# Performance work log

Measured on AMD Instinct MI355X. Metric: run time of the kernel, lower is better.

## Reference

```python
import jax, jax.numpy as jnp
import numpy as np

B, N, C, H = 4, 1024, 768, 12
HD = C // H

def setup_inputs() -> dict:
    key = jax.random.key(0)
    ks = jax.random.split(key, 6)
    s = 0.02
    return {
        "x": jax.random.normal(ks[0], (B, N, C), jnp.float32),
        "attn_bias": jax.random.normal(ks[1], (H, N, N), jnp.float32),
        "qkv_w": jax.random.normal(ks[2], (C, 3 * C), jnp.float32) * s,
        "qkv_b": jax.random.normal(ks[3], (3 * C,), jnp.float32) * s,
        "proj_w": jax.random.normal(ks[4], (C, C), jnp.float32) * s,
        "proj_b": jax.random.normal(ks[5], (C,), jnp.float32) * s,
    }

def reference(x, attn_bias, qkv_w, qkv_b, proj_w, proj_b):
    b, n, c = x.shape
    scale = HD ** -0.5
    qkv = x @ qkv_w + qkv_b                      # [B,N,3C]
    qkv = qkv.reshape(b, n, 3, H, HD)
    q = qkv[:, :, 0].transpose(0, 2, 1, 3)       # [B,H,N,HD]
    k = qkv[:, :, 1].transpose(0, 2, 1, 3)
    v = qkv[:, :, 2].transpose(0, 2, 1, 3)
    attn = jnp.einsum('bhqd,bhkd->bhqk', q, k) * scale
    attn = attn + attn_bias[None]                # broadcast over batch
    attn = jax.nn.softmax(attn, axis=-1)
    y = jnp.einsum('bhqk,bhkd->bhqd', attn, v)   # [B,H,N,HD]
    y = y.transpose(0, 2, 1, 3).reshape(b, n, c)
    return y @ proj_w + proj_b
```

## Files before the change

kernel.cpp:

```cpp
#include <hip/hip_runtime.h>
#include <hip/hip_bf16.h>

constexpr int BATCH = 4;
constexpr int NSEQ  = 1024;
constexpr int CDIM  = 768;
constexpr int NHEAD = 12;
constexpr int HDIM  = 64;
constexpr int MTOT  = BATCH * NSEQ;
constexpr int QKVN  = 3 * CDIM;

typedef __bf16 bf16x8 __attribute__((ext_vector_type(8)));
typedef float  f32x4  __attribute__((ext_vector_type(4)));

__device__ __forceinline__ unsigned short f2bf(float f) {
    unsigned u = __builtin_bit_cast(unsigned, f);
    unsigned r = u + 0x7FFFu + ((u >> 16) & 1u);
    return (unsigned short)(r >> 16);
}

#define GLOAD_LDS16(gp, lp)                                                    \
    __builtin_amdgcn_global_load_lds(                                          \
        (const __attribute__((address_space(1))) void*)(gp),                   \
        (__attribute__((address_space(3))) void*)(lp), 16, 0, 0)

__global__ __launch_bounds__(256) void cvt_f32_bf16(
    const float* __restrict__ in, unsigned short* __restrict__ out, int n4)
{
    int i = blockIdx.x * 256 + threadIdx.x;
    if (i < n4) {
        float4 a = reinterpret_cast<const float4*>(in)[i];
        ushort4 h;
        h.x = f2bf(a.x); h.y = f2bf(a.y); h.z = f2bf(a.z); h.w = f2bf(a.w);
        reinterpret_cast<ushort4*>(out)[i] = h;
    }
}

__global__ __launch_bounds__(256) void tcvt_f32_bf16(
    const float* __restrict__ in, unsigned short* __restrict__ out, int R, int C)
{
    __shared__ unsigned short t[32][33];
    const int c0 = blockIdx.x * 32, r0 = blockIdx.y * 32;
    const int tc = threadIdx.x & 31, tr = threadIdx.x >> 5;
    #pragma unroll
    for (int i = 0; i < 4; i++)
        t[tc][tr + 8 * i] = f2bf(in[(size_t)(r0 + tr + 8 * i) * C + c0 + tc]);
    __syncthreads();
    #pragma unroll
    for (int i = 0; i < 4; i++)
        out[(size_t)(c0 + tr + 8 * i) * R + r0 + tc] = t[tr + 8 * i][tc];
}

__global__ __launch_bounds__(256) void qkv_gemm(
    const unsigned short* __restrict__ xb,
    const unsigned short* __restrict__ wt,
    const float* __restrict__ bias,
    unsigned short* __restrict__ qbuf, unsigned short* __restrict__ kbuf,
    unsigned short* __restrict__ vtbuf)
{
    __shared__ unsigned short As[128 * 32];
    __shared__ unsigned short Bs[128 * 32];
    const int tid  = threadIdx.x;
    const int lane = tid & 63;
    const int wid  = tid >> 6;
    const int wm = (wid >> 1) * 64, wn = (wid & 1) * 64;
    const int g = lane >> 4, li = lane & 15;
    const int m0 = blockIdx.y * 128;
    const int n0 = blockIdx.x * 128;
    const int srow = lane >> 2;
    const int scol = (lane & 3) * 8;

    f32x4 acc[4][4];
    #pragma unroll
    for (int i = 0; i < 4; i++)
        #pragma unroll
        for (int j = 0; j < 4; j++) acc[i][j] = f32x4{0.f, 0.f, 0.f, 0.f};

    for (int k0 = 0; k0 < CDIM; k0 += 32) {
        __syncthreads();
        #pragma unroll
        for (int c = 0; c < 2; c++) {
            int row = wid * 32 + c * 16 + srow;
            GLOAD_LDS16(&xb[(size_t)(m0 + row) * CDIM + k0 + scol],
                        &As[(wid * 32 + c * 16) * 32]);
            GLOAD_LDS16(&wt[(size_t)(n0 + row) * CDIM + k0 + scol],
                        &Bs[(wid * 32 + c * 16) * 32]);
        }
        __syncthreads();
        bf16x8 a[4], b[4];
        #pragma unroll
        for (int mt = 0; mt < 4; mt++)
            a[mt] = *reinterpret_cast<const bf16x8*>(&As[(wm + 16 * mt + li) * 32 + 8 * g]);
        #pragma unroll
        for (int nt = 0; nt < 4; nt++)
            b[nt] = *reinterpret_cast<const bf16x8*>(&Bs[(wn + 16 * nt + li) * 32 + 8 * g]);
        #pragma unroll
        for (int mt = 0; mt < 4; mt++)
            #pragma unroll
            for (int nt = 0; nt < 4; nt++)
                acc[mt][nt] = __builtin_amdgcn_mfma_f32_16x16x32_bf16(a[mt], b[nt], acc[mt][nt], 0, 0, 0);
    }

    #pragma unroll
    for (int mt = 0; mt < 4; mt++) {
        #pragma unroll
        for (int nt = 0; nt < 4; nt++) {
            int col  = n0 + wn + 16 * nt + li;
            int tsel = col / CDIM;
            int rem  = col - tsel * CDIM;
            int h_ = rem >> 6, d = rem & 63;
            float bv = bias[col];
            #pragma unroll
            for (int r = 0; r < 4; r++) {
                int m  = m0 + wm + 16 * mt + 4 * g + r;
                int b_ = m >> 10, s = m & 1023;
                unsigned short hv = f2bf(acc[mt][nt][r] + bv);
                if (tsel == 0)
                    qbuf[(((size_t)b_ * NHEAD + h_) * NSEQ + s) * HDIM + d] = hv;
                else if (tsel == 1)
                    kbuf[(((size_t)b_ * NHEAD + h_) * NSEQ + s) * HDIM + d] = hv;
                else
                    vtbuf[(((size_t)b_ * NHEAD + h_) * HDIM + d) * NSEQ + s] = hv;
            }
        }
    }
}

__global__ __launch_bounds__(256, 3) void attn_kernel(
    const unsigned short* __restrict__ qbuf,
    const unsigned short* __restrict__ kbuf,
    const unsigned short* __restrict__ vtbuf,
    const float* __restrict__ bias,
    unsigned short* __restrict__ ybuf)
{
    __shared__ unsigned short Ks[128][72];
    __shared__ unsigned short Vs[64][136];
    __shared__ unsigned short Ps[4][16][136];

    const int tid  = threadIdx.x;
    const int lane = tid & 63;
    const int wid  = tid >> 6;
    const int g = lane >> 4, li = lane & 15;
    const int bh = blockIdx.y;
    const int b_ = bh / NHEAD, h_ = bh % NHEAD;
    const int qw = blockIdx.x * 64 + wid * 16;
    const float scale = 0.125f;

    const unsigned short* qb = qbuf + (size_t)bh * NSEQ * HDIM;
    const unsigned short* kb = kbuf + (size_t)bh * NSEQ * HDIM;
    const unsigned short* vb = vtbuf + (size_t)bh * HDIM * NSEQ;
    const float* bb = bias + (size_t)h_ * NSEQ * NSEQ;

    bf16x8 qf[2];
    #pragma unroll
    for (int dd = 0; dd < 2; dd++)
        qf[dd] = *reinterpret_cast<const bf16x8*>(&qb[(size_t)(qw + li) * HDIM + 32 * dd + 8 * g]);

    f32x4 oacc[4];
    #pragma unroll
    for (int dt = 0; dt < 4; dt++) oacc[dt] = f32x4{0.f, 0.f, 0.f, 0.f};
    float lpart[4] = {0.f, 0.f, 0.f, 0.f};

    for (int k0 = 0; k0 < NSEQ; k0 += 128) {
        float bv[8][4];
        #pragma unroll
        for (int kt = 0; kt < 8; kt++)
            #pragma unroll
            for (int r = 0; r < 4; r++)
                bv[kt][r] = bb[(size_t)(qw + 4 * g + r) * NSEQ + k0 + 16 * kt + li];

        __syncthreads();
        #pragma unroll
        for (int i = 0; i < 4; i++) {
            int j = tid * 4 + i;
            int row = j >> 3, c = (j & 7) * 8;
            *reinterpret_cast<int4*>(&Ks[row][c]) =
                *reinterpret_cast<const int4*>(&kb[(size_t)(k0 + row) * HDIM + c]);
        }
        #pragma unroll
        for (int i = 0; i < 4; i++) {
            int j = tid * 4 + i;
            int row = j >> 4, c = (j & 15) * 8;
            *reinterpret_cast<int4*>(&Vs[row][c]) =
                *reinterpret_cast<const int4*>(&vb[(size_t)row * NSEQ + k0 + c]);
        }
        __syncthreads();

        f32x4 sacc[8];
        #pragma unroll
        for (int kt = 0; kt < 8; kt++) sacc[kt] = f32x4{0.f, 0.f, 0.f, 0.f};
        #pragma unroll
        for (int kt = 0; kt < 8; kt++)
            #pragma unroll
            for (int dd = 0; dd < 2; dd++) {
                bf16x8 kf = *reinterpret_cast<const bf16x8*>(&Ks[16 * kt + li][32 * dd + 8 * g]);
                sacc[kt] = __builtin_amdgcn_mfma_f32_16x16x32_bf16(qf[dd], kf, sacc[kt], 0, 0, 0);
            }

        #pragma unroll
        for (int kt = 0; kt < 8; kt++)
            #pragma unroll
            for (int r = 0; r < 4; r++) {
                float pv = __expf(sacc[kt][r] * scale + bv[kt][r]);
                lpart[r] += pv;
                Ps[wid][4 * g + r][16 * kt + li] = f2bf(pv);
            }

        #pragma unroll
        for (int kk = 0; kk < 4; kk++) {
            bf16x8 pf = *reinterpret_cast<const bf16x8*>(&Ps[wid][li][32 * kk + 8 * g]);
            #pragma unroll
            for (int dt = 0; dt < 4; dt++) {
                bf16x8 vf = *reinterpret_cast<const bf16x8*>(&Vs[16 * dt + li][32 * kk + 8 * g]);
                oacc[dt] = __builtin_amdgcn_mfma_f32_16x16x32_bf16(pf, vf, oacc[dt], 0, 0, 0);
            }
        }
    }

    float linv[4];
    #pragma unroll
    for (int r = 0; r < 4; r++) {
        float s = lpart[r];
        s += __shfl_xor(s, 1);
        s += __shfl_xor(s, 2);
        s += __shfl_xor(s, 4);
        s += __shfl_xor(s, 8);
        linv[r] = 1.f / s;
    }
    #pragma unroll
    for (int dt = 0; dt < 4; dt++)
        #pragma unroll
        for (int r = 0; r < 4; r++) {
            float o = oacc[dt][r] * linv[r];
            int s = qw + 4 * g + r;
            ybuf[((size_t)b_ * NSEQ + s) * CDIM + h_ * HDIM + 16 * dt + li] = f2bf(o);
        }
}

__global__ __launch_bounds__(256) void proj_gemm(
    const unsigned short* __restrict__ yb,
    const unsigned short* __restrict__ pwt,
    const float* __restrict__ bias, float* __restrict__ out)
{
    __shared__ unsigned short As[128 * 32];
    __shared__ unsigned short Bs[128 * 32];
    const int tid  = threadIdx.x;
    const int lane = tid & 63;
    const int wid  = tid >> 6;
    const int wm = (wid >> 1) * 64, wn = (wid & 1) * 64;
    const int g = lane >> 4, li = lane & 15;
    const int m0 = blockIdx.y * 128;
    const int n0 = blockIdx.x * 128;
    const int srow = lane >> 2;
    const int scol = (lane & 3) * 8;

    f32x4 acc[4][4];
    #pragma unroll
    for (int i = 0; i < 4; i++)
        #pragma unroll
        for (int j = 0; j < 4; j++) acc[i][j] = f32x4{0.f, 0.f, 0.f, 0.f};

    for (int k0 = 0; k0 < CDIM; k0 += 32) {
        __syncthreads();
        #pragma unroll
        for (int c = 0; c < 2; c++) {
            int row = wid * 32 + c * 16 + srow;
            GLOAD_LDS16(&yb[(size_t)(m0 + row) * CDIM + k0 + scol],
                        &As[(wid * 32 + c * 16) * 32]);
            GLOAD_LDS16(&pwt[(size_t)(n0 + row) * CDIM + k0 + scol],
                        &Bs[(wid * 32 + c * 16) * 32]);
        }
        __syncthreads();
        bf16x8 a[4], b[4];
        #pragma unroll
        for (int mt = 0; mt < 4; mt++)
            a[mt] = *reinterpret_cast<const bf16x8*>(&As[(wm + 16 * mt + li) * 32 + 8 * g]);
        #pragma unroll
        for (int nt = 0; nt < 4; nt++)
            b[nt] = *reinterpret_cast<const bf16x8*>(&Bs[(wn + 16 * nt + li) * 32 + 8 * g]);
        #pragma unroll
        for (int mt = 0; mt < 4; mt++)
            #pragma unroll
            for (int nt = 0; nt < 4; nt++)
                acc[mt][nt] = __builtin_amdgcn_mfma_f32_16x16x32_bf16(a[mt], b[nt], acc[mt][nt], 0, 0, 0);
    }

    #pragma unroll
    for (int mt = 0; mt < 4; mt++)
        #pragma unroll
        for (int nt = 0; nt < 4; nt++) {
            int col = n0 + wn + 16 * nt + li;
            float bv = bias[col];
            #pragma unroll
            for (int r = 0; r < 4; r++) {
                int m = m0 + wm + 16 * mt + 4 * g + r;
                out[(size_t)m * CDIM + col] = acc[mt][nt][r] + bv;
            }
        }
}

extern "C" void kernel_launch(void* const* d_in, const int* in_sizes, int n_in,
                              void* d_out, int out_size, void* d_ws, size_t ws_size,
                              hipStream_t stream) {
    const float* x         = (const float*)d_in[0];
    const float* attn_bias = (const float*)d_in[1];
    const float* qkv_w     = (const float*)d_in[2];
    const float* qkv_b     = (const float*)d_in[3];
    const float* proj_w    = (const float*)d_in[4];
    const float* proj_b    = (const float*)d_in[5];
    float* out = (float*)d_out;

    const size_t per = (size_t)BATCH * NHEAD * NSEQ * HDIM;
    unsigned short* qbuf  = (unsigned short*)d_ws;
    unsigned short* kbuf  = qbuf + per;
    unsigned short* vtbuf = kbuf + per;
    unsigned short* xb    = vtbuf + per;
    unsigned short* qwt   = xb + per;
    unsigned short* pwt   = qwt + (size_t)QKVN * CDIM;
    unsigned short* ybuf  = xb;

    cvt_f32_bf16<<<(MTOT * CDIM / 4 + 255) / 256, 256, 0, stream>>>(
        x, xb, MTOT * CDIM / 4);
    tcvt_f32_bf16<<<dim3(QKVN / 32, CDIM / 32), 256, 0, stream>>>(
        qkv_w, qwt, CDIM, QKVN);
    tcvt_f32_bf16<<<dim3(CDIM / 32, CDIM / 32), 256, 0, stream>>>(
        proj_w, pwt, CDIM, CDIM);

    qkv_gemm<<<dim3(QKVN / 128, MTOT / 128), 256, 0, stream>>>(
        xb, qwt, qkv_b, qbuf, kbuf, vtbuf);
    attn_kernel<<<dim3(NSEQ / 64, BATCH * NHEAD), 256, 0, stream>>>(
        qbuf, kbuf, vtbuf, attn_bias, ybuf);
    proj_gemm<<<dim3(CDIM / 128, MTOT / 128), 256, 0, stream>>>(
        ybuf, pwt, proj_b, out);
}
```

Before: 114.2 us.

## Prefetch next K/V/bias tile into registers and swizzle attention block order

The attention kernel now loads the next 128-key tile of K, V and the bias into registers while the current tile's MFMAs run, using double-buffered bias registers and a fully unrolled key loop. The grid becomes a flat 768-block launch with a swizzle that maps consecutive block IDs across different (batch, head) pairs. The swizzle probably spreads work across XCDs so blocks sharing the same head's bias and K/V land together for cache reuse. The cost is much higher register pressure (two 32-float bias sets plus 8 int4 prefetch registers), which may cut occupancy below the launch_bounds target of 3.

```diff
diff --git a/kernel.cpp b/kernel.cpp
--- a/kernel.cpp
+++ b/kernel.cpp
@@ -140,9 +140,13 @@
     const int lane = tid & 63;
     const int wid  = tid >> 6;
     const int g = lane >> 4, li = lane & 15;
-    const int bh = blockIdx.y;
+
+    const int lin = blockIdx.x;
+    const int swz = (lin & 7) * 96 + (lin >> 3);
+    const int qtile = swz & 15;
+    const int bh    = swz >> 4;
     const int b_ = bh / NHEAD, h_ = bh % NHEAD;
-    const int qw = blockIdx.x * 64 + wid * 16;
+    const int qw = qtile * 64 + wid * 16;
     const float scale = 0.125f;
 
     const unsigned short* qb = qbuf + (size_t)bh * NSEQ * HDIM;
@@ -160,30 +164,49 @@
     for (int dt = 0; dt < 4; dt++) oacc[dt] = f32x4{0.f, 0.f, 0.f, 0.f};
     float lpart[4] = {0.f, 0.f, 0.f, 0.f};
 
-    for (int k0 = 0; k0 < NSEQ; k0 += 128) {
-        float bv[8][4];
-        #pragma unroll
-        for (int kt = 0; kt < 8; kt++)
-            #pragma unroll
-            for (int r = 0; r < 4; r++)
-                bv[kt][r] = bb[(size_t)(qw + 4 * g + r) * NSEQ + k0 + 16 * kt + li];
-
-        __syncthreads();
-        #pragma unroll
-        for (int i = 0; i < 4; i++) {
-            int j = tid * 4 + i;
-            int row = j >> 3, c = (j & 7) * 8;
-            *reinterpret_cast<int4*>(&Ks[row][c]) =
-                *reinterpret_cast<const int4*>(&kb[(size_t)(k0 + row) * HDIM + c]);
-        }
-        #pragma unroll
-        for (int i = 0; i < 4; i++) {
-            int j = tid * 4 + i;
-            int row = j >> 4, c = (j & 15) * 8;
-            *reinterpret_cast<int4*>(&Vs[row][c]) =
-                *reinterpret_cast<const int4*>(&vb[(size_t)row * NSEQ + k0 + c]);
-        }
-        __syncthreads();
+    const int krow = tid >> 1, kcol = (tid & 1) * 32;
+    const int vrow = tid >> 2, vcol = (tid & 3) * 32;
+    int4 kreg[4], vreg[4];
+    float bv[2][8][4];
+
+    #pragma unroll
+    for (int i = 0; i < 4; i++) {
+        kreg[i] = *reinterpret_cast<const int4*>(&kb[(size_t)krow * HDIM + kcol + i * 8]);
+        vreg[i] = *reinterpret_cast<const int4*>(&vb[(size_t)vrow * NSEQ + vcol + i * 8]);
+    }
+    #pragma unroll
+    for (int kt = 0; kt < 8; kt++)
+        #pragma unroll
+        for (int r = 0; r < 4; r++)
+            bv[0][kt][r] = bb[(size_t)(qw + 4 * g + r) * NSEQ + 16 * kt + li];
+
+    #pragma unroll
+    for (int t = 0; t < 8; ++t) {
+        const int k0 = t * 128;
+        __syncthreads();
+        #pragma unroll
+        for (int i = 0; i < 4; i++)
+            *reinterpret_cast<int4*>(&Ks[krow][kcol + i * 8]) = kreg[i];
+        #pragma unroll
+        for (int i = 0; i < 4; i++)
+            *reinterpret_cast<int4*>(&Vs[vrow][vcol + i * 8]) = vreg[i];
+        __syncthreads();
+
+        if (t < 7) {
+            #pragma unroll
+            for (int i = 0; i < 4; i++) {
+                kreg[i] = *reinterpret_cast<const int4*>(
+                    &kb[(size_t)(k0 + 128 + krow) * HDIM + kcol + i * 8]);
+                vreg[i] = *reinterpret_cast<const int4*>(
+                    &vb[(size_t)vrow * NSEQ + k0 + 128 + vcol + i * 8]);
+            }
+            #pragma unroll
+            for (int kt = 0; kt < 8; kt++)
+                #pragma unroll
+                for (int r = 0; r < 4; r++)
+                    bv[(t + 1) & 1][kt][r] =
+                        bb[(size_t)(qw + 4 * g + r) * NSEQ + k0 + 128 + 16 * kt + li];
+        }
 
         f32x4 sacc[8];
         #pragma unroll
@@ -200,7 +223,7 @@
         for (int kt = 0; kt < 8; kt++)
             #pragma unroll
             for (int r = 0; r < 4; r++) {
-                float pv = __expf(sacc[kt][r] * scale + bv[kt][r]);
+                float pv = __expf(sacc[kt][r] * scale + bv[t & 1][kt][r]);
                 lpart[r] += pv;
                 Ps[wid][4 * g + r][16 * kt + li] = f2bf(pv);
             }
@@ -327,7 +350,7 @@
 
     qkv_gemm<<<dim3(QKVN / 128, MTOT / 128), 256, 0, stream>>>(
         xb, qwt, qkv_b, qbuf, kbuf, vtbuf);
-    attn_kernel<<<dim3(NSEQ / 64, BATCH * NHEAD), 256, 0, stream>>>(
+    attn_kernel<<<768, 256, 0, stream>>>(
         qbuf, kbuf, vtbuf, attn_bias, ybuf);
     proj_gemm<<<dim3(CDIM / 128, MTOT / 128), 256, 0, stream>>>(
         ybuf, pwt, proj_b, out);
```

Result: slower. 231.6 us (+102.8%).

## Transpose S tile for vectorized bias loads and remap blocks for bias reuse

Applied to the files above, without the earlier changes.

Swaps the MFMA operand order so each lane owns one query row and four consecutive keys. The bias can then be read as float4 vectors and P written as packed ushort4 stores, and the row-sum reduction drops to two cross-group shuffles. The grid is flattened and remapped so the four batch instances sharing a head's bias tile run close together, which should improve L2/MALL reuse of the large fp32 bias. The mapping hardcodes 768 blocks and 8-way XCD interleaving, and adds a shuffle-based gather of the row sums.

```diff
diff --git a/kernel.cpp b/kernel.cpp
--- a/kernel.cpp
+++ b/kernel.cpp
@@ -140,9 +140,15 @@
     const int lane = tid & 63;
     const int wid  = tid >> 6;
     const int g = lane >> 4, li = lane & 15;
-    const int bh = blockIdx.y;
-    const int b_ = bh / NHEAD, h_ = bh % NHEAD;
-    const int qw = blockIdx.x * 64 + wid * 16;
+
+    const int lin = blockIdx.x;
+    const int s   = (lin & 7) * 96 + (lin >> 3);
+    const int b_    = s & 3;
+    const int hq    = s >> 2;
+    const int qtile = hq & 15;
+    const int h_    = hq >> 4;
+    const int bh    = b_ * NHEAD + h_;
+    const int qw = qtile * 64 + wid * 16;
     const float scale = 0.125f;
 
     const unsigned short* qb = qbuf + (size_t)bh * NSEQ * HDIM;
@@ -158,15 +164,14 @@
     f32x4 oacc[4];
     #pragma unroll
     for (int dt = 0; dt < 4; dt++) oacc[dt] = f32x4{0.f, 0.f, 0.f, 0.f};
-    float lpart[4] = {0.f, 0.f, 0.f, 0.f};
+    float lpart = 0.f;
 
     for (int k0 = 0; k0 < NSEQ; k0 += 128) {
-        float bv[8][4];
+        f32x4 bv[8];
         #pragma unroll
         for (int kt = 0; kt < 8; kt++)
-            #pragma unroll
-            for (int r = 0; r < 4; r++)
-                bv[kt][r] = bb[(size_t)(qw + 4 * g + r) * NSEQ + k0 + 16 * kt + li];
+            bv[kt] = *reinterpret_cast<const f32x4*>(
+                &bb[(size_t)(qw + li) * NSEQ + k0 + 16 * kt + 4 * g]);
 
         __syncthreads();
         #pragma unroll
@@ -193,17 +198,20 @@
             #pragma unroll
             for (int dd = 0; dd < 2; dd++) {
                 bf16x8 kf = *reinterpret_cast<const bf16x8*>(&Ks[16 * kt + li][32 * dd + 8 * g]);
-                sacc[kt] = __builtin_amdgcn_mfma_f32_16x16x32_bf16(qf[dd], kf, sacc[kt], 0, 0, 0);
+                sacc[kt] = __builtin_amdgcn_mfma_f32_16x16x32_bf16(kf, qf[dd], sacc[kt], 0, 0, 0);
             }
 
         #pragma unroll
-        for (int kt = 0; kt < 8; kt++)
-            #pragma unroll
-            for (int r = 0; r < 4; r++) {
-                float pv = __expf(sacc[kt][r] * scale + bv[kt][r]);
-                lpart[r] += pv;
-                Ps[wid][4 * g + r][16 * kt + li] = f2bf(pv);
-            }
+        for (int kt = 0; kt < 8; kt++) {
+            ushort4 pk;
+            float p0 = __expf(sacc[kt][0] * scale + bv[kt][0]);
+            float p1 = __expf(sacc[kt][1] * scale + bv[kt][1]);
+            float p2 = __expf(sacc[kt][2] * scale + bv[kt][2]);
+            float p3 = __expf(sacc[kt][3] * scale + bv[kt][3]);
+            lpart += p0 + p1 + p2 + p3;
+            pk.x = f2bf(p0); pk.y = f2bf(p1); pk.z = f2bf(p2); pk.w = f2bf(p3);
+            *reinterpret_cast<ushort4*>(&Ps[wid][li][16 * kt + 4 * g]) = pk;
+        }
 
         #pragma unroll
         for (int kk = 0; kk < 4; kk++) {
@@ -216,23 +224,20 @@
         }
     }
 
+    lpart += __shfl_xor(lpart, 16);
+    lpart += __shfl_xor(lpart, 32);
     float linv[4];
     #pragma unroll
-    for (int r = 0; r < 4; r++) {
-        float s = lpart[r];
-        s += __shfl_xor(s, 1);
-        s += __shfl_xor(s, 2);
-        s += __shfl_xor(s, 4);
-        s += __shfl_xor(s, 8);
-        linv[r] = 1.f / s;
-    }
+    for (int r = 0; r < 4; r++)
+        linv[r] = 1.f / __shfl(lpart, 4 * g + r);
+
     #pragma unroll
     for (int dt = 0; dt < 4; dt++)
         #pragma unroll
         for (int r = 0; r < 4; r++) {
             float o = oacc[dt][r] * linv[r];
-            int s = qw + 4 * g + r;
-            ybuf[((size_t)b_ * NSEQ + s) * CDIM + h_ * HDIM + 16 * dt + li] = f2bf(o);
+            int sq = qw + 4 * g + r;
+            ybuf[((size_t)b_ * NSEQ + sq) * CDIM + h_ * HDIM + 16 * dt + li] = f2bf(o);
         }
 }
 
@@ -327,7 +332,7 @@
 
     qkv_gemm<<<dim3(QKVN / 128, MTOT / 128), 256, 0, stream>>>(
         xb, qwt, qkv_b, qbuf, kbuf, vtbuf);
-    attn_kernel<<<dim3(NSEQ / 64, BATCH * NHEAD), 256, 0, stream>>>(
+    attn_kernel<<<768, 256, 0, stream>>>(
         qbuf, kbuf, vtbuf, attn_bias, ybuf);
     proj_gemm<<<dim3(CDIM / 128, MTOT / 128), 256, 0, stream>>>(
         ybuf, pwt, proj_b, out);
```

Measured after the change: 119.3 us. +4.5%, slower.

## Compute transposed scores to keep P in registers and drop LDS round-trip

Applied to the files above, without the earlier changes.

The attention kernel now computes S^T (K as the A operand, Q as B), so each lane's score accumulators line up with the A-operand layout of the P·V MFMA. P is packed to bf16 in registers instead of going through the shared Ps buffer. K rows are permuted when stored to LDS so the transposed layout matches. The softmax scale is folded into Q in the QKV GEMM epilogue, the bias loads become vectorized f32x4 reads along rows, and occupancy is raised to 4 blocks per SM. Together these remove LDS traffic and per-element scale multiplies, at the cost of a tricky lane/row permutation that must exactly match the MFMA operand layout.

```diff
diff --git a/kernel.cpp b/kernel.cpp
--- a/kernel.cpp
+++ b/kernel.cpp
@@ -16,6 +16,10 @@
     unsigned u = __builtin_bit_cast(unsigned, f);
     unsigned r = u + 0x7FFFu + ((u >> 16) & 1u);
     return (unsigned short)(r >> 16);
+}
+
+__device__ __forceinline__ unsigned pack_bf16(float lo, float hi) {
+    return (unsigned)f2bf(lo) | ((unsigned)f2bf(hi) << 16);
 }
 
 #define GLOAD_LDS16(gp, lp)                                                    \
@@ -109,11 +113,12 @@
             int rem  = col - tsel * CDIM;
             int h_ = rem >> 6, d = rem & 63;
             float bv = bias[col];
+            float sc = (tsel == 0) ? 0.125f : 1.0f;
             #pragma unroll
             for (int r = 0; r < 4; r++) {
                 int m  = m0 + wm + 16 * mt + 4 * g + r;
                 int b_ = m >> 10, s = m & 1023;
-                unsigned short hv = f2bf(acc[mt][nt][r] + bv);
+                unsigned short hv = f2bf((acc[mt][nt][r] + bv) * sc);
                 if (tsel == 0)
                     qbuf[(((size_t)b_ * NHEAD + h_) * NSEQ + s) * HDIM + d] = hv;
                 else if (tsel == 1)
@@ -125,16 +130,15 @@
     }
 }
 
-__global__ __launch_bounds__(256, 3) void attn_kernel(
+__global__ __launch_bounds__(256, 4) void attn_kernel(
     const unsigned short* __restrict__ qbuf,
     const unsigned short* __restrict__ kbuf,
     const unsigned short* __restrict__ vtbuf,
     const float* __restrict__ bias,
     unsigned short* __restrict__ ybuf)
 {
-    __shared__ unsigned short Ks[128][72];
-    __shared__ unsigned short Vs[64][136];
-    __shared__ unsigned short Ps[4][16][136];
+    __shared__ unsigned short Ks[128 * 72];
+    __shared__ unsigned short Vs[64 * 136];
 
     const int tid  = threadIdx.x;
     const int lane = tid & 63;
@@ -143,13 +147,25 @@
     const int bh = blockIdx.y;
     const int b_ = bh / NHEAD, h_ = bh % NHEAD;
     const int qw = blockIdx.x * 64 + wid * 16;
-    const float scale = 0.125f;
 
     const unsigned short* qb = qbuf + (size_t)bh * NSEQ * HDIM;
     const unsigned short* kb = kbuf + (size_t)bh * NSEQ * HDIM;
     const unsigned short* vb = vtbuf + (size_t)bh * HDIM * NSEQ;
     const float* bb = bias + (size_t)h_ * NSEQ * NSEQ;
 
+    int ksrc[4], ksoff[4], vsrc[4], vsoff[4];
+    #pragma unroll
+    for (int i = 0; i < 4; i++) {
+        int j = tid * 4 + i;
+        int kr = j >> 3, kc = (j & 7) * 8;
+        int kp = (kr & 0x63) | ((kr & 4) << 2) | ((kr & 0x18) >> 1);
+        ksrc[i] = kr * HDIM + kc;
+        ksoff[i] = kp * 72 + kc;
+        int vr = j >> 4, vc = (j & 15) * 8;
+        vsrc[i] = vr * NSEQ + vc;
+        vsoff[i] = vr * 136 + vc;
+    }
+
     bf16x8 qf[2];
     #pragma unroll
     for (int dd = 0; dd < 2; dd++)
@@ -158,81 +174,78 @@
     f32x4 oacc[4];
     #pragma unroll
     for (int dt = 0; dt < 4; dt++) oacc[dt] = f32x4{0.f, 0.f, 0.f, 0.f};
-    float lpart[4] = {0.f, 0.f, 0.f, 0.f};
+    float lpart = 0.f;
 
     for (int k0 = 0; k0 < NSEQ; k0 += 128) {
-        float bv[8][4];
-        #pragma unroll
-        for (int kt = 0; kt < 8; kt++)
-            #pragma unroll
-            for (int r = 0; r < 4; r++)
-                bv[kt][r] = bb[(size_t)(qw + 4 * g + r) * NSEQ + k0 + 16 * kt + li];
+        f32x4 bvlo[4], bvhi[4];
+        #pragma unroll
+        for (int kk = 0; kk < 4; kk++) {
+            const float* bp = &bb[(size_t)(qw + li) * NSEQ + k0 + 32 * kk + 8 * g];
+            bvlo[kk] = *reinterpret_cast<const f32x4*>(bp);
+            bvhi[kk] = *reinterpret_cast<const f32x4*>(bp + 4);
+        }
 
         __syncthreads();
         #pragma unroll
         for (int i = 0; i < 4; i++) {
-            int j = tid * 4 + i;
-            int row = j >> 3, c = (j & 7) * 8;
-            *reinterpret_cast<int4*>(&Ks[row][c]) =
-                *reinterpret_cast<const int4*>(&kb[(size_t)(k0 + row) * HDIM + c]);
-        }
-        #pragma unroll
-        for (int i = 0; i < 4; i++) {
-            int j = tid * 4 + i;
-            int row = j >> 4, c = (j & 15) * 8;
-            *reinterpret_cast<int4*>(&Vs[row][c]) =
-                *reinterpret_cast<const int4*>(&vb[(size_t)row * NSEQ + k0 + c]);
-        }
-        __syncthreads();
-
-        f32x4 sacc[8];
-        #pragma unroll
-        for (int kt = 0; kt < 8; kt++) sacc[kt] = f32x4{0.f, 0.f, 0.f, 0.f};
-        #pragma unroll
-        for (int kt = 0; kt < 8; kt++)
+            *reinterpret_cast<int4*>(&Ks[ksoff[i]]) =
+                *reinterpret_cast<const int4*>(&kb[(size_t)k0 * HDIM + ksrc[i]]);
+            *reinterpret_cast<int4*>(&Vs[vsoff[i]]) =
+                *reinterpret_cast<const int4*>(&vb[(size_t)k0 + vsrc[i]]);
+        }
+        __syncthreads();
+
+        #pragma unroll
+        for (int kk = 0; kk < 4; kk++) {
+            f32x4 s0 = f32x4{0.f, 0.f, 0.f, 0.f};
+            f32x4 s1 = f32x4{0.f, 0.f, 0.f, 0.f};
             #pragma unroll
             for (int dd = 0; dd < 2; dd++) {
-                bf16x8 kf = *reinterpret_cast<const bf16x8*>(&Ks[16 * kt + li][32 * dd + 8 * g]);
-                sacc[kt] = __builtin_amdgcn_mfma_f32_16x16x32_bf16(qf[dd], kf, sacc[kt], 0, 0, 0);
+                bf16x8 kf0 = *reinterpret_cast<const bf16x8*>(
+                    &Ks[(32 * kk + li) * 72 + 32 * dd + 8 * g]);
+                bf16x8 kf1 = *reinterpret_cast<const bf16x8*>(
+                    &Ks[(32 * kk + 16 + li) * 72 + 32 * dd + 8 * g]);
+                s0 = __builtin_amdgcn_mfma_f32_16x16x32_bf16(kf0, qf[dd], s0, 0, 0, 0);
+                s1 = __builtin_amdgcn_mfma_f32_16x16x32_bf16(kf1, qf[dd], s1, 0, 0, 0);
             }
-
-        #pragma unroll
-        for (int kt = 0; kt < 8; kt++)
-            #pragma unroll
-            for (int r = 0; r < 4; r++) {
-                float pv = __expf(sacc[kt][r] * scale + bv[kt][r]);
-                lpart[r] += pv;
-                Ps[wid][4 * g + r][16 * kt + li] = f2bf(pv);
-            }
-
-        #pragma unroll
-        for (int kk = 0; kk < 4; kk++) {
-            bf16x8 pf = *reinterpret_cast<const bf16x8*>(&Ps[wid][li][32 * kk + 8 * g]);
+            float p0 = __expf(s0[0] + bvlo[kk][0]);
+            float p1 = __expf(s0[1] + bvlo[kk][1]);
+            float p2 = __expf(s0[2] + bvlo[kk][2]);
+            float p3 = __expf(s0[3] + bvlo[kk][3]);
+            float p4 = __expf(s1[0] + bvhi[kk][0]);
+            float p5 = __expf(s1[1] + bvhi[kk][1]);
+            float p6 = __expf(s1[2] + bvhi[kk][2]);
+            float p7 = __expf(s1[3] + bvhi[kk][3]);
+            lpart += ((p0 + p1) + (p2 + p3)) + ((p4 + p5) + (p6 + p7));
+            uint4 pw;
+            pw.x = pack_bf16(p0, p1);
+            pw.y = pack_bf16(p2, p3);
+            pw.z = pack_bf16(p4, p5);
+            pw.w = pack_bf16(p6, p7);
+            bf16x8 pf = __builtin_bit_cast(bf16x8, pw);
             #pragma unroll
             for (int dt = 0; dt < 4; dt++) {
-                bf16x8 vf = *reinterpret_cast<const bf16x8*>(&Vs[16 * dt + li][32 * kk + 8 * g]);
+                bf16x8 vf = *reinterpret_cast<const bf16x8*>(
+                    &Vs[(16 * dt + li) * 136 + 32 * kk + 8 * g]);
                 oacc[dt] = __builtin_amdgcn_mfma_f32_16x16x32_bf16(pf, vf, oacc[dt], 0, 0, 0);
             }
         }
     }
 
+    lpart += __shfl_xor(lpart, 16);
+    lpart += __shfl_xor(lpart, 32);
     float linv[4];
     #pragma unroll
-    for (int r = 0; r < 4; r++) {
-        float s = lpart[r];
-        s += __shfl_xor(s, 1);
-        s += __shfl_xor(s, 2);
-        s += __shfl_xor(s, 4);
-        s += __shfl_xor(s, 8);
-        linv[r] = 1.f / s;
-    }
+    for (int r = 0; r < 4; r++)
+        linv[r] = 1.f / __shfl(lpart, 4 * g + r);
+
     #pragma unroll
     for (int dt = 0; dt < 4; dt++)
         #pragma unroll
         for (int r = 0; r < 4; r++) {
             float o = oacc[dt][r] * linv[r];
-            int s = qw + 4 * g + r;
-            ybuf[((size_t)b_ * NSEQ + s) * CDIM + h_ * HDIM + 16 * dt + li] = f2bf(o);
+            int sq = qw + 4 * g + r;
+            ybuf[((size_t)b_ * NSEQ + sq) * CDIM + h_ * HDIM + 16 * dt + li] = f2bf(o);
         }
 }
 
```

Result: slower. 129.7 us (+13.5%).
